# Optimization experiments

Measured on AMD Instinct MI355X. Metric: run time of the kernel, lower is better.

Reference implementation:

```python
import jax, jax.numpy as jnp
import numpy as np

BLOCK_SIZE = 256
EMB = 384
HEAD = 64
B = 256
T = 256

def setup_inputs() -> dict:
    key = jax.random.key(0)
    k1, k2, k3, k4 = jax.random.split(key, 4)
    x = jax.random.normal(k1, (B, T, EMB), dtype=jnp.float32)
    # torch Linear(no bias) default init ~ U(-1/sqrt(in), 1/sqrt(in)); use scaled normal
    s = 1.0 / np.sqrt(EMB)
    Wq = jax.random.normal(k2, (EMB, HEAD), dtype=jnp.float32) * s
    Wk = jax.random.normal(k3, (EMB, HEAD), dtype=jnp.float32) * s
    Wv = jax.random.normal(k4, (EMB, HEAD), dtype=jnp.float32) * s
    return {"x": x, "Wq": Wq, "Wk": Wk, "Wv": Wv}

def reference(x, Wq, Wk, Wv):
    Bb, Tt, C = x.shape
    q = jnp.einsum('btc,ch->bth', x, Wq)
    k = jnp.einsum('btc,ch->bth', x, Wk)
    v = jnp.einsum('btc,ch->bth', x, Wv)
    # NOTE: source scales by C**-0.5 where C = embedding dim (384), not head_size
    scores = jnp.einsum('bth,bsh->bts', q, k) * (C ** -0.5)  # [B,T,T]
    causal = jnp.tril(jnp.ones((Tt, Tt), dtype=bool))
    scores = jnp.where(causal, scores, -jnp.inf)
    weights = jax.nn.softmax(scores, axis=-1)
    # dropout is identity in eval mode (reference baseline)
    out = jnp.einsum('bts,bsh->bth', weights, v)
    return out
```

## Files before the change

### kernel.cpp

```cpp
#include <hip/hip_runtime.h>
#include <hip/hip_bf16.h>
#include <cstdint>
#include <cstddef>

#define B_DIM 256
#define T_DIM 256
#define EMB   384
#define HEAD  64

typedef __attribute__((ext_vector_type(8))) short bf16x8;
typedef __attribute__((ext_vector_type(4))) float f32x4;
typedef __attribute__((ext_vector_type(4))) unsigned int u32x4;

__device__ __forceinline__ unsigned short f2bf(float f) {
    union { float f; unsigned int u; } v; v.f = f;
    unsigned int r = v.u + 0x7fffu + ((v.u >> 16) & 1u);
    return (unsigned short)(r >> 16);
}

__device__ __forceinline__ unsigned int pkbf(float a, float b) {
#if __has_builtin(__builtin_amdgcn_cvt_pk_bf16_f32)
    typedef __attribute__((ext_vector_type(2))) __bf16 bf16x2_t;
    bf16x2_t r = __builtin_amdgcn_cvt_pk_bf16_f32(a, b);
    return *(unsigned int*)&r;
#else
    return (unsigned)f2bf(a) | ((unsigned)f2bf(b) << 16);
#endif
}

__global__ void wprep_kernel(const float* __restrict__ Wq, const float* __restrict__ Wk,
                             const float* __restrict__ Wv, unsigned short* __restrict__ Wb) {
    int g = blockIdx.x * blockDim.x + threadIdx.x;
    if (g >= 9216) return;
    int kkstep = g / 1536, rem = g - kkstep * 1536;
    int r = rem >> 3, cs = rem & 7, c = cs ^ (r & 7);
    const float* W = (r < 64) ? Wq : (r < 128) ? Wk : Wv;
    int h = r & 63;
#pragma unroll
    for (int e = 0; e < 8; ++e) {
        int k = kkstep * 64 + c * 8 + e;
        Wb[(size_t)g * 8 + e] = f2bf(W[k * HEAD + h]);
    }
}

__global__ __launch_bounds__(512, 2) void fused_kernel(const float* __restrict__ x,
                                                       const unsigned short* __restrict__ Wb,
                                                       float* __restrict__ out) {
    __shared__ union SM {
        struct { unsigned short Xs[256][72]; unsigned short Ws[2][12288]; } p1;
        struct { unsigned short qs[256][72]; unsigned short ks[256][72];
                 unsigned short vT[64][264]; unsigned short Ps[8][16][72]; } p2;
    } sm;

    const int tid = threadIdx.x;
    const int w = tid >> 6, lane = tid & 63, qd = lane >> 4, l15 = lane & 15;
    const int mh = w >> 1, nh = w & 1;
    const int b = blockIdx.x;
    const float* xb = x + (size_t)b * T_DIM * EMB;

    f32x4 acc[4][6];
#pragma unroll
    for (int mt = 0; mt < 4; ++mt)
#pragma unroll
        for (int nt = 0; nt < 6; ++nt) acc[mt][nt] = (f32x4){0.f, 0.f, 0.f, 0.f};

    float4 xr[8];
#pragma unroll
    for (int s = 0; s < 3; ++s) {
        int idx = s * 512 + w * 64;
        const unsigned short* gp = Wb + (size_t)(idx + lane) * 8;
        unsigned short* lp = &sm.p1.Ws[0][idx * 8];
        __builtin_amdgcn_global_load_lds(
            (const __attribute__((address_space(1))) unsigned int*)gp,
            (__attribute__((address_space(3))) unsigned int*)lp, 16, 0, 0);
    }
#pragma unroll
    for (int s = 0; s < 8; ++s) {
        int i = tid + 512 * s;
        int row = i >> 4, c4 = (i & 15) << 2;
        xr[s] = *(const float4*)(xb + (size_t)row * EMB + c4);
    }

    for (int kk = 0; kk < 6; ++kk) {
        __syncthreads();
#pragma unroll
        for (int s = 0; s < 8; ++s) {
            int i = tid + 512 * s;
            int row = i >> 4, c4 = (i & 15) << 2;
            *(uint2*)&sm.p1.Xs[row][c4] = make_uint2(pkbf(xr[s].x, xr[s].y), pkbf(xr[s].z, xr[s].w));
        }
        __syncthreads();
        if (kk < 5) {
#pragma unroll
            for (int s = 0; s < 3; ++s) {
                int idx = s * 512 + w * 64;
                const unsigned short* gp = Wb + (size_t)((kk + 1) * 1536 + idx + lane) * 8;
                unsigned short* lp = &sm.p1.Ws[(kk + 1) & 1][idx * 8];
                __builtin_amdgcn_global_load_lds(
                    (const __attribute__((address_space(1))) unsigned int*)gp,
                    (__attribute__((address_space(3))) unsigned int*)lp, 16, 0, 0);
            }
#pragma unroll
            for (int s = 0; s < 8; ++s) {
                int i = tid + 512 * s;
                int row = i >> 4, c4 = (i & 15) << 2;
                xr[s] = *(const float4*)(xb + (size_t)row * EMB + (kk + 1) * 64 + c4);
            }
        }
#pragma unroll
        for (int kb = 0; kb < 2; ++kb) {
            bf16x8 a[4], bb[6];
#pragma unroll
            for (int mt = 0; mt < 4; ++mt)
                a[mt] = *(const bf16x8*)&sm.p1.Xs[64 * mh + 16 * mt + l15][32 * kb + 8 * qd];
#pragma unroll
            for (int nt = 0; nt < 6; ++nt) {
                int n = 96 * nh + 16 * nt + l15;
                bb[nt] = *(const bf16x8*)&sm.p1.Ws[kk & 1][n * 64 + (((4 * kb + qd) ^ (n & 7)) << 3)];
            }
#pragma unroll
            for (int mt = 0; mt < 4; ++mt)
#pragma unroll
                for (int nt = 0; nt < 6; ++nt)
                    acc[mt][nt] = __builtin_amdgcn_mfma_f32_16x16x32_bf16(a[mt], bb[nt], acc[mt][nt], 0, 0, 0);
        }
    }
    __syncthreads();

#pragma unroll
    for (int nt = 0; nt < 6; ++nt) {
        int n = 96 * nh + 16 * nt + l15;
        int arr = n >> 6, h = n & 63;
#pragma unroll
        for (int mt = 0; mt < 4; ++mt)
#pragma unroll
            for (int reg = 0; reg < 4; ++reg) {
                int tok = 64 * mh + 16 * mt + 4 * qd + reg;
                unsigned short val = f2bf(acc[mt][nt][reg]);
                if (arr == 0)      sm.p2.qs[tok][h] = val;
                else if (arr == 1) sm.p2.ks[tok][h] = val;
                else               sm.p2.vT[h][tok] = val;
            }
    }
    __syncthreads();

    const int tiles[2] = { w, 15 - w };
    bf16x8 aq[2][2];
#pragma unroll
    for (int ti = 0; ti < 2; ++ti)
#pragma unroll
        for (int kbi = 0; kbi < 2; ++kbi)
            aq[ti][kbi] = *(const bf16x8*)&sm.p2.qs[16 * tiles[ti] + l15][32 * kbi + 8 * qd];

    f32x4 O[2][4];
    float l[2][4];
#pragma unroll
    for (int ti = 0; ti < 2; ++ti) {
#pragma unroll
        for (int dn = 0; dn < 4; ++dn) O[ti][dn] = (f32x4){0.f, 0.f, 0.f, 0.f};
#pragma unroll
        for (int reg = 0; reg < 4; ++reg) l[ti][reg] = 0.f;
    }

    const float cExp = 1.4426950408889634f / 19.595917942265423f;

#pragma unroll
    for (int ti = 0; ti < 2; ++ti) {
        const int t = tiles[ti];
        for (int jc = 0; jc <= (t >> 2); ++jc) {
            const int ntmax = min(3, t - 4 * jc);
            f32x4 S[4];
#pragma unroll
            for (int nt = 0; nt < 4; ++nt) {
                if (nt <= ntmax) {
                    bf16x8 b0 = *(const bf16x8*)&sm.p2.ks[64 * jc + 16 * nt + l15][8 * qd];
                    bf16x8 b1 = *(const bf16x8*)&sm.p2.ks[64 * jc + 16 * nt + l15][32 + 8 * qd];
                    f32x4 s = __builtin_amdgcn_mfma_f32_16x16x32_bf16(aq[ti][0], b0, (f32x4){0.f,0.f,0.f,0.f}, 0, 0, 0);
                    s = __builtin_amdgcn_mfma_f32_16x16x32_bf16(aq[ti][1], b1, s, 0, 0, 0);
                    S[nt] = s;
                }
            }
#pragma unroll
            for (int nt = 0; nt < 4; ++nt) {
#pragma unroll
                for (int reg = 0; reg < 4; ++reg) {
                    float p = 0.0f;
                    if (nt <= ntmax) {
                        p = exp2f(S[nt][reg] * cExp);
                        if (4 * jc + nt == t && (l15 > 4 * qd + reg)) p = 0.0f;
                    }
                    l[ti][reg] += p;
                    sm.p2.Ps[w][4 * qd + reg][16 * nt + l15] = f2bf(p);
                }
            }
            bf16x8 ap0 = *(const bf16x8*)&sm.p2.Ps[w][l15][8 * qd];
            bf16x8 ap1 = *(const bf16x8*)&sm.p2.Ps[w][l15][32 + 8 * qd];
#pragma unroll
            for (int dn = 0; dn < 4; ++dn) {
                bf16x8 bv0 = *(const bf16x8*)&sm.p2.vT[16 * dn + l15][64 * jc + 8 * qd];
                bf16x8 bv1 = *(const bf16x8*)&sm.p2.vT[16 * dn + l15][64 * jc + 32 + 8 * qd];
                O[ti][dn] = __builtin_amdgcn_mfma_f32_16x16x32_bf16(ap0, bv0, O[ti][dn], 0, 0, 0);
                O[ti][dn] = __builtin_amdgcn_mfma_f32_16x16x32_bf16(ap1, bv1, O[ti][dn], 0, 0, 0);
            }
        }
    }

#pragma unroll
    for (int ti = 0; ti < 2; ++ti) {
#pragma unroll
        for (int reg = 0; reg < 4; ++reg) {
            float s = l[ti][reg];
            s += __shfl_xor(s, 1);
            s += __shfl_xor(s, 2);
            s += __shfl_xor(s, 4);
            s += __shfl_xor(s, 8);
            float inv = 1.0f / s;
            int row = 16 * tiles[ti] + 4 * qd + reg;
            float* dst = out + ((size_t)b * T_DIM + row) * HEAD;
#pragma unroll
            for (int dn = 0; dn < 4; ++dn)
                dst[16 * dn + l15] = O[ti][dn][reg] * inv;
        }
    }
}

extern "C" void kernel_launch(void* const* d_in, const int* in_sizes, int n_in,
                              void* d_out, int out_size, void* d_ws, size_t ws_size,
                              hipStream_t stream) {
    const float* x  = (const float*)d_in[0];
    const float* Wq = (const float*)d_in[1];
    const float* Wk = (const float*)d_in[2];
    const float* Wv = (const float*)d_in[3];
    float* out = (float*)d_out;

    unsigned short* Wb = (unsigned short*)d_ws;

    wprep_kernel<<<36, 256, 0, stream>>>(Wq, Wk, Wv, Wb);
    fused_kernel<<<B_DIM, 512, 0, stream>>>(x, Wb, out);
}
```

Baseline: 174.6 us.

## Double-buffer X tile in LDS and vectorize V-transpose and weight-prep stores

Double-buffers the bf16 X staging tile in shared memory so the next K-step's X tile is written after the MFMA loop, removing one __syncthreads per iteration. V results are now written to the transposed LDS array as packed 4-element bf16 stores instead of scalar shorts. The weight-prep kernel now writes each group of eight bf16 values with one 16-byte store. Shared memory in phase 1 grows by one 256x72 bf16 buffer, which could affect occupancy at two blocks per CU.

```diff
diff --git a/kernel.cpp b/kernel.cpp
--- a/kernel.cpp
+++ b/kernel.cpp
@@ -36,18 +36,20 @@
     int r = rem >> 3, cs = rem & 7, c = cs ^ (r & 7);
     const float* W = (r < 64) ? Wq : (r < 128) ? Wk : Wv;
     int h = r & 63;
+    unsigned short tmp[8];
 #pragma unroll
     for (int e = 0; e < 8; ++e) {
         int k = kkstep * 64 + c * 8 + e;
-        Wb[(size_t)g * 8 + e] = f2bf(W[k * HEAD + h]);
-    }
+        tmp[e] = f2bf(W[k * HEAD + h]);
+    }
+    *(u32x4*)(Wb + (size_t)g * 8) = *(u32x4*)tmp;
 }
 
 __global__ __launch_bounds__(512, 2) void fused_kernel(const float* __restrict__ x,
                                                        const unsigned short* __restrict__ Wb,
                                                        float* __restrict__ out) {
     __shared__ union SM {
-        struct { unsigned short Xs[256][72]; unsigned short Ws[2][12288]; } p1;
+        struct { unsigned short Xs[2][256][72]; unsigned short Ws[2][12288]; } p1;
         struct { unsigned short qs[256][72]; unsigned short ks[256][72];
                  unsigned short vT[64][264]; unsigned short Ps[8][16][72]; } p2;
     } sm;
@@ -57,6 +59,7 @@
     const int mh = w >> 1, nh = w & 1;
     const int b = blockIdx.x;
     const float* xb = x + (size_t)b * T_DIM * EMB;
+    const int xrow = tid >> 4, xc4 = (tid & 15) << 2;
 
     f32x4 acc[4][6];
 #pragma unroll
@@ -75,20 +78,13 @@
             (__attribute__((address_space(3))) unsigned int*)lp, 16, 0, 0);
     }
 #pragma unroll
-    for (int s = 0; s < 8; ++s) {
-        int i = tid + 512 * s;
-        int row = i >> 4, c4 = (i & 15) << 2;
-        xr[s] = *(const float4*)(xb + (size_t)row * EMB + c4);
-    }
+    for (int s = 0; s < 8; ++s)
+        xr[s] = *(const float4*)(xb + (size_t)(xrow + 32 * s) * EMB + xc4);
+#pragma unroll
+    for (int s = 0; s < 8; ++s)
+        *(uint2*)&sm.p1.Xs[0][xrow + 32 * s][xc4] = make_uint2(pkbf(xr[s].x, xr[s].y), pkbf(xr[s].z, xr[s].w));
 
     for (int kk = 0; kk < 6; ++kk) {
-        __syncthreads();
-#pragma unroll
-        for (int s = 0; s < 8; ++s) {
-            int i = tid + 512 * s;
-            int row = i >> 4, c4 = (i & 15) << 2;
-            *(uint2*)&sm.p1.Xs[row][c4] = make_uint2(pkbf(xr[s].x, xr[s].y), pkbf(xr[s].z, xr[s].w));
-        }
         __syncthreads();
         if (kk < 5) {
 #pragma unroll
@@ -101,18 +97,15 @@
                     (__attribute__((address_space(3))) unsigned int*)lp, 16, 0, 0);
             }
 #pragma unroll
-            for (int s = 0; s < 8; ++s) {
-                int i = tid + 512 * s;
-                int row = i >> 4, c4 = (i & 15) << 2;
-                xr[s] = *(const float4*)(xb + (size_t)row * EMB + (kk + 1) * 64 + c4);
-            }
+            for (int s = 0; s < 8; ++s)
+                xr[s] = *(const float4*)(xb + (size_t)(xrow + 32 * s) * EMB + (kk + 1) * 64 + xc4);
         }
 #pragma unroll
         for (int kb = 0; kb < 2; ++kb) {
             bf16x8 a[4], bb[6];
 #pragma unroll
             for (int mt = 0; mt < 4; ++mt)
-                a[mt] = *(const bf16x8*)&sm.p1.Xs[64 * mh + 16 * mt + l15][32 * kb + 8 * qd];
+                a[mt] = *(const bf16x8*)&sm.p1.Xs[kk & 1][64 * mh + 16 * mt + l15][32 * kb + 8 * qd];
 #pragma unroll
             for (int nt = 0; nt < 6; ++nt) {
                 int n = 96 * nh + 16 * nt + l15;
@@ -124,6 +117,12 @@
                 for (int nt = 0; nt < 6; ++nt)
                     acc[mt][nt] = __builtin_amdgcn_mfma_f32_16x16x32_bf16(a[mt], bb[nt], acc[mt][nt], 0, 0, 0);
         }
+        if (kk < 5) {
+#pragma unroll
+            for (int s = 0; s < 8; ++s)
+                *(uint2*)&sm.p1.Xs[(kk + 1) & 1][xrow + 32 * s][xc4] =
+                    make_uint2(pkbf(xr[s].x, xr[s].y), pkbf(xr[s].z, xr[s].w));
+        }
     }
     __syncthreads();
 
@@ -131,16 +130,25 @@
     for (int nt = 0; nt < 6; ++nt) {
         int n = 96 * nh + 16 * nt + l15;
         int arr = n >> 6, h = n & 63;
-#pragma unroll
-        for (int mt = 0; mt < 4; ++mt)
-#pragma unroll
-            for (int reg = 0; reg < 4; ++reg) {
-                int tok = 64 * mh + 16 * mt + 4 * qd + reg;
-                unsigned short val = f2bf(acc[mt][nt][reg]);
-                if (arr == 0)      sm.p2.qs[tok][h] = val;
-                else if (arr == 1) sm.p2.ks[tok][h] = val;
-                else               sm.p2.vT[h][tok] = val;
-            }
+        if (arr == 2) {
+#pragma unroll
+            for (int mt = 0; mt < 4; ++mt) {
+                int tok0 = 64 * mh + 16 * mt + 4 * qd;
+                *(uint2*)&sm.p2.vT[h][tok0] = make_uint2(
+                    pkbf(acc[mt][nt][0], acc[mt][nt][1]),
+                    pkbf(acc[mt][nt][2], acc[mt][nt][3]));
+            }
+        } else {
+#pragma unroll
+            for (int mt = 0; mt < 4; ++mt)
+#pragma unroll
+                for (int reg = 0; reg < 4; ++reg) {
+                    int tok = 64 * mh + 16 * mt + 4 * qd + reg;
+                    unsigned short val = f2bf(acc[mt][nt][reg]);
+                    if (arr == 0) sm.p2.qs[tok][h] = val;
+                    else          sm.p2.ks[tok][h] = val;
+                }
+        }
     }
     __syncthreads();
 
```

New measurement: 171.4 us. About the same (-1.8%).
